# Kernel optimization log

Measured on AMD Instinct MI355X. Metric: run time of the kernel, lower is better.

The kernel has to match this reference:

```python
import jax, jax.numpy as jnp
import numpy as np

B, S, D, H = 2, 2048, 1024, 16
HD = D // H
EPS = 1e-8
LN_EPS = 1e-5


def setup_inputs() -> dict:
    key = jax.random.key(0)
    ks = jax.random.split(key, 12)
    std = 0.02
    inp = {}
    inp["x"] = jax.random.normal(ks[0], (B, S, D), jnp.float32)
    # q/k/v/out projections (stored (in, out); y = x @ W + b)
    inp["Wq"] = jax.random.normal(ks[1], (D, D), jnp.float32) * std
    inp["bq"] = jnp.zeros((D,), jnp.float32)
    inp["Wk"] = jax.random.normal(ks[2], (D, D), jnp.float32) * std
    inp["bk"] = jnp.zeros((D,), jnp.float32)
    inp["Wv"] = jax.random.normal(ks[3], (D, D), jnp.float32) * std
    inp["bv"] = jnp.zeros((D,), jnp.float32)
    inp["Wo"] = jax.random.normal(ks[4], (D, D), jnp.float32) * std
    inp["bo"] = jnp.zeros((D,), jnp.float32)
    # 4 DeltaResidualBlocks stacked on axis 0: [q, k, v, out]
    inp["dWk"] = jax.random.normal(ks[5], (4, D, D), jnp.float32) * 0.01  # k_proj, no bias
    inp["dbw"] = jnp.zeros((4, D), jnp.float32)                           # beta_proj weight (init zeros)
    inp["dbb"] = jnp.full((4,), -4.0, jnp.float32)                        # beta_proj bias
    inp["dWv"] = jax.random.normal(ks[6], (4, D), jnp.float32) * 0.02     # v_proj weight (d_v=1)
    inp["dbv"] = jnp.zeros((4,), jnp.float32)                             # v_proj bias
    inp["ln_g"] = jnp.ones((D,), jnp.float32)
    inp["ln_b"] = jnp.zeros((D,), jnp.float32)
    return inp


def reference(x, Wq, bq, Wk, bk, Wv, bv, Wo, bo, dWk, dbw, dbb, dWv, dbv, ln_g, ln_b):
    def delta(h, v_in, i):
        # DeltaResidualBlock (d_v=1): h + beta * k * (v - k.h)
        k_raw = jnp.einsum('bsd,de->bse', h, dWk[i])
        k = k_raw / (jnp.linalg.norm(k_raw, axis=-1, keepdims=True) + EPS)
        beta = 2.0 * jax.nn.sigmoid(jnp.einsum('bsd,d->bs', h, dbw[i])[..., None] + dbb[i])  # (B,S,1)
        v = jnp.einsum('bsd,d->bs', v_in, dWv[i])[..., None] + dbv[i]                        # (B,S,1)
        k_dot_h = jnp.sum(k * h, axis=-1, keepdims=True)
        return h + beta * k * (v - k_dot_h)

    q = delta(x, x @ Wq + bq, 0)
    k = delta(x, x @ Wk + bk, 1)
    v = delta(x, x @ Wv + bv, 2)

    # (B,S,D) -> (B,H,S,HD)
    q = q.reshape(B, S, H, HD).transpose(0, 2, 1, 3)
    k = k.reshape(B, S, H, HD).transpose(0, 2, 1, 3)
    v = v.reshape(B, S, H, HD).transpose(0, 2, 1, 3)

    scale = HD ** -0.5
    scores = jnp.einsum('bhqd,bhkd->bhqk', q, k) * scale
    attn = jax.nn.softmax(scores, axis=-1)
    out = jnp.einsum('bhqk,bhkd->bhqd', attn, v)
    out = out.transpose(0, 2, 1, 3).reshape(B, S, D)
    out = out @ Wo + bo

    y = delta(x, out, 3)

    # LayerNorm
    mu = jnp.mean(y, axis=-1, keepdims=True)
    var = jnp.mean((y - mu) ** 2, axis=-1, keepdims=True)
    y = (y - mu) / jnp.sqrt(var + LN_EPS) * ln_g + ln_b
    return y
```

## Files before the change

### kernel.cpp

```cpp
#include <hip/hip_runtime.h>

#define BB 2
#define SS 2048
#define DD 1024
#define HH 16
#define HD 64
#define MM (BB*SS)
#define KC 4
#define KT_PER (SS/64/KC)

typedef unsigned short u16;
typedef __attribute__((ext_vector_type(8))) short bf16x8;
typedef __attribute__((ext_vector_type(4))) float f32x4;

typedef __attribute__((address_space(1))) const unsigned int* gas_t;
typedef __attribute__((address_space(3))) unsigned int* las_t;

#ifndef __has_builtin
#define __has_builtin(x) 0
#endif
#if __has_builtin(__builtin_amdgcn_exp2f)
#define EXP2F(x) __builtin_amdgcn_exp2f(x)
#else
#define EXP2F(x) __expf((x)*0.6931471805599453f)
#endif
#define QSCALE 0.18033688011112042f

__device__ __forceinline__ void gl_lds16(const u16* g, u16* l){
  __builtin_amdgcn_global_load_lds((gas_t)g, (las_t)l, 16, 0, 0);
}

__device__ __forceinline__ u16 f2bf(float f){
  unsigned u = __float_as_uint(f);
  u += 0x7FFF + ((u >> 16) & 1);
  return (u16)(u >> 16);
}
__device__ __forceinline__ float bf2f(u16 h){
  return __uint_as_float(((unsigned)h) << 16);
}
__device__ __forceinline__ float dot4f(float4 a, float4 b){
  return a.x*b.x + a.y*b.y + a.z*b.z + a.w*b.w;
}

#define NB_CONV 2048
#define NB_TRAN 2048
#define NB_PREC 4100
#define NB_PREP (NB_CONV+NB_TRAN+NB_PREC)
__global__ void prep_kernel(const float* __restrict__ x, u16* __restrict__ xb,
                            const float* __restrict__ dWk, u16* __restrict__ dWkT,
                            const float* __restrict__ Wq_, const float* __restrict__ bq_,
                            const float* __restrict__ Wk_, const float* __restrict__ bk_,
                            const float* __restrict__ Wv_, const float* __restrict__ bv_,
                            const float* __restrict__ Wo_, const float* __restrict__ bo_,
                            const float* __restrict__ dWv, const float* __restrict__ dbv,
                            float* __restrict__ wv, float* __restrict__ cv) {
  int blk = blockIdx.x, t = threadIdx.x;
  if (blk < NB_CONV) {
    size_t idx = ((size_t)blk*256 + t)*8;
    float4 a = *(const float4*)(x + idx);
    float4 b = *(const float4*)(x + idx + 4);
    union { u16 u[8]; uint4 v; } pk;
    pk.u[0]=f2bf(a.x); pk.u[1]=f2bf(a.y); pk.u[2]=f2bf(a.z); pk.u[3]=f2bf(a.w);
    pk.u[4]=f2bf(b.x); pk.u[5]=f2bf(b.y); pk.u[6]=f2bf(b.z); pk.u[7]=f2bf(b.w);
    *(uint4*)(xb + idx) = pk.v;
    return;
  }
  blk -= NB_CONV;
  if (blk < NB_TRAN) {
    int xi = blk & 3, rest = blk >> 2;
    int ck = rest & 127, i = rest >> 7;
    int n  = xi*256 + t;
    const float* src = dWk + (size_t)i*DD*DD + (size_t)ck*8*DD + n;
    union { u16 u[8]; uint4 v; } pk;
    #pragma unroll
    for (int e=0;e<8;e++) pk.u[e] = f2bf(src[(size_t)e*DD]);
    *(uint4*)(dWkT + (size_t)i*DD*DD + (size_t)n*DD + ck*8) = pk.v;
    return;
  }
  blk -= NB_TRAN;
  {
    int i = blk / 1025, row = blk % 1025;
    const float* W    = (i==0)?Wq_:(i==1)?Wk_:(i==2)?Wv_:Wo_;
    const float* bvec = (i==0)?bq_:(i==1)?bk_:(i==2)?bv_:bo_;
    const float* s = dWv + i*DD;
    __shared__ float red[256];
    float acc = 0.f;
    if (row < DD) {
      const float* r = W + (size_t)row * DD;
      for (int e = t; e < DD; e += 256) acc += r[e]*s[e];
    } else {
      for (int e = t; e < DD; e += 256) acc += bvec[e]*s[e];
    }
    red[t] = acc; __syncthreads();
    for (int off=128; off>0; off>>=1){ if(t<off) red[t]+=red[t+off]; __syncthreads(); }
    if (t==0) {
      if (row < DD) wv[i*DD + row] = red[0];
      else          cv[i] = red[0] + dbv[i];
    }
  }
}

__global__ __launch_bounds__(256) void gemm_dwk_mfma(const u16* __restrict__ xb,
                          const u16* __restrict__ Bt, u16* __restrict__ kraw) {
  const int id = blockIdx.x;
  const int xcd = id & 7, j = id >> 3;
  const int i = j & 3, rest = j >> 2;
  const int mloc = rest & 7, nloc = rest >> 3;
  const int m0 = ((((xcd & 3) << 3) | mloc) << 7);
  const int n0 = ((((xcd >> 2) << 2) | nloc) << 7);
  const u16* Bm = Bt + (size_t)i*DD*DD;
  u16* C = kraw + (size_t)i*MM*DD;
  const int t = threadIdx.x, w = t>>6, lane = t&63;
  const int q15 = lane&15, quad = lane>>4;
  const int wm = w>>1, wn = w&1;
  const int lr = lane>>3, lc = lane&7, gsw = lc ^ lr;
  const int sw = q15 & 7;
  __shared__ u16 As[128*64];
  __shared__ u16 Bs[128*64];
  f32x4 acc[4][4];
  #pragma unroll
  for(int a=0;a<4;a++)
    #pragma unroll
    for(int b2=0;b2<4;b2++) acc[a][b2] = (f32x4){0.f,0.f,0.f,0.f};

  for (int k0=0; k0<DD; k0+=64) {
    __syncthreads();
    #pragma unroll
    for (int j2=0; j2<4; j2++) {
      int r = (w*4+j2)*8 + lr;
      gl_lds16(xb + (size_t)(m0+r)*DD + k0 + gsw*8, &As[((w*4+j2)*8)*64]);
      gl_lds16(Bm + (size_t)(n0+r)*DD + k0 + gsw*8, &Bs[((w*4+j2)*8)*64]);
    }
    __syncthreads();
    #pragma unroll
    for (int kk=0; kk<2; kk++) {
      bf16x8 af[4], bfr[4];
      #pragma unroll
      for (int mt=0; mt<4; mt++)
        af[mt]  = *(bf16x8*)(&As[(wm*64+mt*16+q15)*64 + ((kk*4+quad)^sw)*8]);
      #pragma unroll
      for (int nt=0; nt<4; nt++)
        bfr[nt] = *(bf16x8*)(&Bs[(wn*64+nt*16+q15)*64 + ((kk*4+quad)^sw)*8]);
      #pragma unroll
      for (int mt=0; mt<4; mt++)
        #pragma unroll
        for (int nt=0; nt<4; nt++)
          acc[mt][nt] = __builtin_amdgcn_mfma_f32_16x16x32_bf16(af[mt], bfr[nt], acc[mt][nt], 0,0,0);
    }
  }
  #pragma unroll
  for (int mt=0; mt<4; mt++)
    #pragma unroll
    for (int nt=0; nt<4; nt++)
      #pragma unroll
      for (int r=0; r<4; r++) {
        int m = m0 + wm*64 + mt*16 + quad*4 + r;
        int n = n0 + wn*64 + nt*16 + q15;
        C[(size_t)m*DD + n] = f2bf(acc[mt][nt][r]);
      }
}

__global__ void delta_qkv_kernel(const float* __restrict__ x, const u16* __restrict__ kraw,
                                 const float* __restrict__ dbw, const float* __restrict__ dbb,
                                 const float* __restrict__ wv, const float* __restrict__ cv,
                                 u16* __restrict__ qk, float* __restrict__ Vw) {
  int m = blockIdx.x, t = threadIdx.x, w = t>>6, lane = t&63;
  const float* xr = x + (size_t)m*DD;
  float4 xv = *(const float4*)(xr + t*4);
  __shared__ float4 part[3][4];
  float4 kvs[3];
  #pragma unroll
  for (int i=0;i<3;i++) {
    ushort4 ku = *(const ushort4*)(kraw + (size_t)i*MM*DD + (size_t)m*DD + t*4);
    float4 kv = make_float4(bf2f(ku.x), bf2f(ku.y), bf2f(ku.z), bf2f(ku.w));
    kvs[i] = kv;
    float4 bwv = *(const float4*)(dbw + i*DD + t*4);
    float4 wvv = *(const float4*)(wv  + i*DD + t*4);
    float4 red = make_float4(dot4f(kv,kv), dot4f(kv,xv), dot4f(xv,bwv), dot4f(xv,wvv));
    #pragma unroll
    for (int off=32; off>0; off>>=1) {
      red.x += __shfl_xor(red.x, off);
      red.y += __shfl_xor(red.y, off);
      red.z += __shfl_xor(red.z, off);
      red.w += __shfl_xor(red.w, off);
    }
    if (lane==0) part[i][w] = red;
  }
  __syncthreads();
  float cc[3];
  #pragma unroll
  for (int i=0;i<3;i++) {
    float4 r0=part[i][0], r1=part[i][1], r2=part[i][2], r3=part[i][3];
    float s0=r0.x+r1.x+r2.x+r3.x, s1=r0.y+r1.y+r2.y+r3.y;
    float s2=r0.z+r1.z+r2.z+r3.z, s3=r0.w+r1.w+r2.w+r3.w;
    float nrmE = sqrtf(s0) + 1e-8f;
    float kdh  = s1 / nrmE;
    float beta = 2.f / (1.f + __expf(-(s2 + dbb[i])));
    float vs   = s3 + cv[i];
    cc[i] = beta * (vs - kdh) / nrmE;
  }
  {
    float c = cc[0]; float4 kv = kvs[0];
    ushort4 ou;
    ou.x = f2bf((xv.x + c*kv.x)*QSCALE); ou.y = f2bf((xv.y + c*kv.y)*QSCALE);
    ou.z = f2bf((xv.z + c*kv.z)*QSCALE); ou.w = f2bf((xv.w + c*kv.w)*QSCALE);
    *(ushort4*)(qk + (size_t)m*DD + t*4) = ou;
  }
  {
    float c = cc[1]; float4 kv = kvs[1];
    ushort4 ou;
    ou.x = f2bf(xv.x + c*kv.x); ou.y = f2bf(xv.y + c*kv.y);
    ou.z = f2bf(xv.z + c*kv.z); ou.w = f2bf(xv.w + c*kv.w);
    *(ushort4*)(qk + (size_t)MM*DD + (size_t)m*DD + t*4) = ou;
  }
  {
    float c = cc[2]; float4 kv = kvs[2];
    float4 vv = make_float4(xv.x + c*kv.x, xv.y + c*kv.y, xv.z + c*kv.z, xv.w + c*kv.w);
    float4 w3 = *(const float4*)(wv + 3*DD + t*4);
    float s = dot4f(vv, w3);
    #pragma unroll
    for (int off=1; off<16; off<<=1) s += __shfl_xor(s, off);
    if ((lane & 15) == 0) {
      int head = t >> 4;
      int b = m >> 11, srow = m & (SS-1);
      Vw[((size_t)(b*HH + head))*SS + srow] = s;
    }
  }
}

__global__ __launch_bounds__(256) void flash_mfma(const u16* __restrict__ qb,
     const u16* __restrict__ kb, const float* __restrict__ Vw,
     float* __restrict__ l_arr, float* __restrict__ pv_arr) {
  const int qt = blockIdx.x, h = blockIdx.y;
  const int b = blockIdx.z >> 2, kc = blockIdx.z & 3;
  const int t = threadIdx.x, w = t>>6, lane = t&63, q15 = lane&15, quad = lane>>4;
  const int lr = lane>>3, lc = lane&7, gsw = lc ^ lr;
  const int sw = q15 & 7;
  __shared__ u16 Qs[64*64];
  __shared__ u16 Ks[2][64*64];
  const size_t hb = (size_t)h*HD;
  const u16* kbase = kb + (size_t)(b*SS + kc*KT_PER*64)*DD + hb;
  const float* vwb = Vw + (size_t)(b*HH + h)*SS + kc*KT_PER*64;

  #pragma unroll
  for (int j=0; j<2; j++) {
    int r = (w*2+j)*8 + lr;
    gl_lds16(qb + (size_t)(b*SS + qt*64 + r)*DD + hb + gsw*8, &Qs[((w*2+j)*8)*64]);
    gl_lds16(kbase + (size_t)r*DD + gsw*8, &Ks[0][((w*2+j)*8)*64]);
  }
  float4 vwreg[4];
  #pragma unroll
  for (int rt=0; rt<4; rt++) vwreg[rt] = *(const float4*)(vwb + rt*16 + quad*4);

  float l_acc = 0.f, pv_acc = 0.f;
  __syncthreads();
  bf16x8 qf[2];
  #pragma unroll
  for (int kk=0; kk<2; kk++)
    qf[kk] = *(bf16x8*)(&Qs[(w*16+q15)*64 + ((kk*4+quad)^sw)*8]);

  for (int kt=0; kt<KT_PER; kt++) {
    if (kt+1 < KT_PER) {
      #pragma unroll
      for (int j=0; j<2; j++) {
        int r = (w*2+j)*8 + lr;
        gl_lds16(kbase + (size_t)((kt+1)*64 + r)*DD + gsw*8,
                 &Ks[(kt+1)&1][((w*2+j)*8)*64]);
      }
    }
    f32x4 Sacc[4];
    #pragma unroll
    for (int rt=0; rt<4; rt++) Sacc[rt] = (f32x4){0.f,0.f,0.f,0.f};
    #pragma unroll
    for (int kk=0; kk<2; kk++) {
      #pragma unroll
      for (int rt=0; rt<4; rt++) {
        bf16x8 kf = *(bf16x8*)(&Ks[kt&1][(rt*16+q15)*64 + ((kk*4+quad)^sw)*8]);
        Sacc[rt] = __builtin_amdgcn_mfma_f32_16x16x32_bf16(kf, qf[kk], Sacc[rt], 0,0,0);
      }
    }
    float4 vwcur[4];
    #pragma unroll
    for (int rt=0; rt<4; rt++) vwcur[rt] = vwreg[rt];
    if (kt+1 < KT_PER) {
      #pragma unroll
      for (int rt=0; rt<4; rt++)
        vwreg[rt] = *(const float4*)(vwb + (kt+1)*64 + rt*16 + quad*4);
    }
    #pragma unroll
    for (int rt=0; rt<4; rt++) {
      float va[4] = {vwcur[rt].x, vwcur[rt].y, vwcur[rt].z, vwcur[rt].w};
      #pragma unroll
      for (int r=0; r<4; r++) {
        float p = EXP2F(fminf(Sacc[rt][r], 30.f));
        l_acc  += p;
        pv_acc += p * va[r];
      }
    }
    __syncthreads();
  }
  l_acc  += __shfl_xor(l_acc, 16);  l_acc  += __shfl_xor(l_acc, 32);
  pv_acc += __shfl_xor(pv_acc, 16); pv_acc += __shfl_xor(pv_acc, 32);
  if (quad == 0) {
    int tok = b*SS + qt*64 + w*16 + q15;
    size_t idx = ((size_t)kc*MM + tok)*HH + h;
    l_arr[idx]  = l_acc;
    pv_arr[idx] = pv_acc;
  }
}

__global__ void final_kernel(const float* __restrict__ x, const u16* __restrict__ kraw3,
                             const float* __restrict__ l_arr, const float* __restrict__ pv_arr,
                             const float* __restrict__ dbw, const float* __restrict__ dbb,
                             const float* __restrict__ cv,
                             const float* __restrict__ ln_g, const float* __restrict__ ln_b,
                             float* __restrict__ out) {
  int m = blockIdx.x, t = threadIdx.x, w = t>>6, lane = t&63;
  const float* xr = x     + (size_t)m*DD;
  const u16*   kr = kraw3 + (size_t)m*DD;
  float4 xv  = *(const float4*)(xr + t*4);
  ushort4 ku = *(const ushort4*)(kr + t*4);
  float4 kv  = make_float4(bf2f(ku.x), bf2f(ku.y), bf2f(ku.z), bf2f(ku.w));
  float4 bwv = *(const float4*)(dbw + 3*DD + t*4);
  __shared__ float4 part[4];
  __shared__ float2 part2[4];
  __shared__ float v3s;
  if (t < 16) {
    float lsum = 0.f, psum = 0.f;
    #pragma unroll
    for (int kc=0; kc<KC; kc++) {
      size_t idx = ((size_t)kc*MM + m)*HH + t;
      lsum += l_arr[idx];
      psum += pv_arr[idx];
    }
    float val = psum / lsum;
    #pragma unroll
    for (int off=1; off<16; off<<=1) val += __shfl_xor(val, off);
    if (t==0) v3s = val;
  }
  float4 red = make_float4(dot4f(kv,kv), dot4f(kv,xv), dot4f(xv,bwv), 0.f);
  #pragma unroll
  for (int off=32; off>0; off>>=1) {
    red.x += __shfl_xor(red.x, off);
    red.y += __shfl_xor(red.y, off);
    red.z += __shfl_xor(red.z, off);
  }
  if (lane==0) part[w] = red;
  __syncthreads();
  float4 r0=part[0], r1=part[1], r2=part[2], r3=part[3];
  float s0=r0.x+r1.x+r2.x+r3.x, s1=r0.y+r1.y+r2.y+r3.y, s2=r0.z+r1.z+r2.z+r3.z;
  float nrmE = sqrtf(s0) + 1e-8f;
  float kdh  = s1 / nrmE;
  float beta = 2.f / (1.f + __expf(-(s2 + dbb[3])));
  float v3   = v3s + cv[3];
  float c = beta * (v3 - kdh) / nrmE;
  float y0 = xv.x + c*kv.x, y1 = xv.y + c*kv.y, y2 = xv.z + c*kv.z, y3 = xv.w + c*kv.w;
  float2 rr = make_float2(y0+y1+y2+y3, y0*y0+y1*y1+y2*y2+y3*y3);
  #pragma unroll
  for (int off=32; off>0; off>>=1) {
    rr.x += __shfl_xor(rr.x, off);
    rr.y += __shfl_xor(rr.y, off);
  }
  if (lane==0) part2[w] = rr;
  __syncthreads();
  float ssum = part2[0].x+part2[1].x+part2[2].x+part2[3].x;
  float ssq  = part2[0].y+part2[1].y+part2[2].y+part2[3].y;
  float mu   = ssum * (1.f/DD);
  float var  = ssq * (1.f/DD) - mu*mu;
  float rstd = rsqrtf(var + 1e-5f);
  float4 g  = *(const float4*)(ln_g + t*4);
  float4 bb = *(const float4*)(ln_b + t*4);
  float4 ov;
  ov.x = (y0-mu)*rstd*g.x + bb.x;
  ov.y = (y1-mu)*rstd*g.y + bb.y;
  ov.z = (y2-mu)*rstd*g.z + bb.z;
  ov.w = (y3-mu)*rstd*g.w + bb.w;
  *(float4*)(out + (size_t)m*DD + t*4) = ov;
}

extern "C" void kernel_launch(void* const* d_in, const int* in_sizes, int n_in,
                              void* d_out, int out_size, void* d_ws, size_t ws_size,
                              hipStream_t stream) {
  const float* x    = (const float*)d_in[0];
  const float* Wq_  = (const float*)d_in[1];
  const float* bq_  = (const float*)d_in[2];
  const float* Wk_  = (const float*)d_in[3];
  const float* bk_  = (const float*)d_in[4];
  const float* Wv_  = (const float*)d_in[5];
  const float* bv_  = (const float*)d_in[6];
  const float* Wo_  = (const float*)d_in[7];
  const float* bo_  = (const float*)d_in[8];
  const float* dWk  = (const float*)d_in[9];
  const float* dbw  = (const float*)d_in[10];
  const float* dbb  = (const float*)d_in[11];
  const float* dWv  = (const float*)d_in[12];
  const float* dbv  = (const float*)d_in[13];
  const float* ln_g = (const float*)d_in[14];
  const float* ln_b = (const float*)d_in[15];
  float* out = (float*)d_out;
  char* WS = (char*)d_ws;

  float* wv     = (float*)WS;
  float* cv     = (float*)(WS + 16384);
  u16*   kraw   = (u16*)  (WS + 16640);
  u16*   qk     = (u16*)  (WS + 16640 + (size_t)4*MM*DD*2);
  u16*   dWkT   = (u16*)  (WS + 16640 + (size_t)6*MM*DD*2);
  u16*   xb     = (u16*)  (WS + 16640 + (size_t)6*MM*DD*2 + (size_t)4*DD*DD*2);
  char*  tail   = WS + 16640 + (size_t)6*MM*DD*2 + (size_t)8*DD*DD*2;
  float* Vw     = (float*)tail;
  float* l_arr  = (float*)(tail + (size_t)BB*HH*SS*4);
  float* pv_arr = (float*)(tail + (size_t)BB*HH*SS*4 + (size_t)KC*MM*HH*4);

  prep_kernel<<<NB_PREP, 256, 0, stream>>>(
      x, xb, dWk, dWkT, Wq_,bq_,Wk_,bk_,Wv_,bv_,Wo_,bo_, dWv, dbv, wv, cv);
  gemm_dwk_mfma<<<1024, 256, 0, stream>>>(xb, dWkT, kraw);
  delta_qkv_kernel<<<MM, 256, 0, stream>>>(x, kraw, dbw, dbb, wv, cv, qk, Vw);
  flash_mfma<<<dim3(SS/64, HH, BB*KC), 256, 0, stream>>>(
      qk, qk + (size_t)MM*DD, Vw, l_arr, pv_arr);
  final_kernel<<<MM, 256, 0, stream>>>(x, kraw + 3*(size_t)MM*DD, l_arr, pv_arr,
                                       dbw, dbb, cv, ln_g, ln_b, out);
}
```

Measured before the change: 236.7 us.

## Rewrite delta-key GEMM as 256x256 tile, double-buffered 8-phase pipelined kernel

Replaces the 128x128, single-buffered delta k_proj GEMM with a 256x256 tile kernel using 512 threads and two LDS buffers. Global-to-LDS loads for later k-steps are issued in halves between four MFMA phases, with explicit vmcnt waits, scheduling barriers and setprio to overlap memory with matrix math. The larger tile raises data reuse, and the grid shrinks to 256 blocks with a new XCD-aware mapping. This costs much more LDS and register pressure, leaves fewer blocks for load balancing, and relies on hand-tuned wait counts being correct.

```diff
diff --git a/kernel.cpp b/kernel.cpp
--- a/kernel.cpp
+++ b/kernel.cpp
@@ -8,6 +8,7 @@
 #define MM (BB*SS)
 #define KC 4
 #define KT_PER (SS/64/KC)
+#define KSTEPS (DD/64)
 
 typedef unsigned short u16;
 typedef __attribute__((ext_vector_type(8))) short bf16x8;
@@ -41,6 +42,12 @@
 __device__ __forceinline__ float dot4f(float4 a, float4 b){
   return a.x*b.x + a.y*b.y + a.z*b.z + a.w*b.w;
 }
+
+#define SBAR() do { \
+  __builtin_amdgcn_sched_barrier(0); \
+  __builtin_amdgcn_s_barrier(); \
+  __builtin_amdgcn_sched_barrier(0); \
+} while (0)
 
 #define NB_CONV 2048
 #define NB_TRAN 2048
@@ -100,63 +107,128 @@
   }
 }
 
-__global__ __launch_bounds__(256) void gemm_dwk_mfma(const u16* __restrict__ xb,
+
+__device__ __forceinline__ void stage_half(const u16* __restrict__ g, u16* l,
+                                           int k0, int half, int isA,
+                                           int wid, int lane) {
+  const int lr = lane>>3, lc = lane&7;
+  #pragma unroll
+  for (int j=0; j<2; j++) {
+    const int u = wid*2 + j;
+    int grow;
+    if (isA) grow = ((u & 8) ? 128 + ((u & 7)<<3) : (u<<3)) + (half<<6);
+    else     grow = ((u>>2)<<6) + ((u&3)<<3) + (half<<5);
+    gl_lds16(g + (size_t)(grow + lr)*DD + k0 + ((lc^lr)<<3), l + grow*64);
+  }
+}
+
+__device__ __forceinline__ void lda4(const u16* base, int row0, int q15, int quad,
+                                     int sw, bf16x8 (&f)[4][2]) {
+  #pragma unroll
+  for (int mf=0; mf<4; mf++)
+    #pragma unroll
+    for (int kk=0; kk<2; kk++)
+      f[mf][kk] = *(const bf16x8*)(base + (row0 + mf*16 + q15)*64 + (((kk*4+quad)^sw)<<3));
+}
+__device__ __forceinline__ void ldb2(const u16* base, int row0, int q15, int quad,
+                                     int sw, bf16x8 (&f)[2][2]) {
+  #pragma unroll
+  for (int nf=0; nf<2; nf++)
+    #pragma unroll
+    for (int kk=0; kk<2; kk++)
+      f[nf][kk] = *(const bf16x8*)(base + (row0 + nf*16 + q15)*64 + (((kk*4+quad)^sw)<<3));
+}
+__device__ __forceinline__ void quad_mfma(const bf16x8 (&af)[4][2], const bf16x8 (&bfr)[2][2],
+                                          f32x4 (&acc)[8][4], int mo, int no) {
+  __builtin_amdgcn_s_setprio(1);
+  #pragma unroll
+  for (int kk=0; kk<2; kk++)
+    #pragma unroll
+    for (int mf=0; mf<4; mf++)
+      #pragma unroll
+      for (int nf=0; nf<2; nf++)
+        acc[mo+mf][no+nf] = __builtin_amdgcn_mfma_f32_16x16x32_bf16(
+            af[mf][kk], bfr[nf][kk], acc[mo+mf][no+nf], 0,0,0);
+  __builtin_amdgcn_s_setprio(0);
+}
+
+__global__ __launch_bounds__(512, 2) void gemm_dwk_8ph(const u16* __restrict__ xb,
                           const u16* __restrict__ Bt, u16* __restrict__ kraw) {
-  const int id = blockIdx.x;
-  const int xcd = id & 7, j = id >> 3;
-  const int i = j & 3, rest = j >> 2;
-  const int mloc = rest & 7, nloc = rest >> 3;
-  const int m0 = ((((xcd & 3) << 3) | mloc) << 7);
-  const int n0 = ((((xcd >> 2) << 2) | nloc) << 7);
-  const u16* Bm = Bt + (size_t)i*DD*DD;
+  const int bid = blockIdx.x;
+  const int xcd = bid & 7, rr = bid >> 3;
+  const int i = xcd >> 1;
+  const int mt = ((xcd & 1) << 3) | (rr & 7);
+  const int ntile = rr >> 3;
+  const int m0 = mt << 8, n0 = ntile << 8;
+  const u16* Ab = xb + (size_t)m0*DD;
+  const u16* Bb = Bt + (size_t)i*DD*DD + (size_t)n0*DD;
   u16* C = kraw + (size_t)i*MM*DD;
-  const int t = threadIdx.x, w = t>>6, lane = t&63;
-  const int q15 = lane&15, quad = lane>>4;
-  const int wm = w>>1, wn = w&1;
-  const int lr = lane>>3, lc = lane&7, gsw = lc ^ lr;
-  const int sw = q15 & 7;
-  __shared__ u16 As[128*64];
-  __shared__ u16 Bs[128*64];
-  f32x4 acc[4][4];
-  #pragma unroll
-  for(int a=0;a<4;a++)
-    #pragma unroll
-    for(int b2=0;b2<4;b2++) acc[a][b2] = (f32x4){0.f,0.f,0.f,0.f};
-
-  for (int k0=0; k0<DD; k0+=64) {
-    __syncthreads();
-    #pragma unroll
-    for (int j2=0; j2<4; j2++) {
-      int r = (w*4+j2)*8 + lr;
-      gl_lds16(xb + (size_t)(m0+r)*DD + k0 + gsw*8, &As[((w*4+j2)*8)*64]);
-      gl_lds16(Bm + (size_t)(n0+r)*DD + k0 + gsw*8, &Bs[((w*4+j2)*8)*64]);
-    }
-    __syncthreads();
-    #pragma unroll
-    for (int kk=0; kk<2; kk++) {
-      bf16x8 af[4], bfr[4];
-      #pragma unroll
-      for (int mt=0; mt<4; mt++)
-        af[mt]  = *(bf16x8*)(&As[(wm*64+mt*16+q15)*64 + ((kk*4+quad)^sw)*8]);
-      #pragma unroll
-      for (int nt=0; nt<4; nt++)
-        bfr[nt] = *(bf16x8*)(&Bs[(wn*64+nt*16+q15)*64 + ((kk*4+quad)^sw)*8]);
-      #pragma unroll
-      for (int mt=0; mt<4; mt++)
-        #pragma unroll
-        for (int nt=0; nt<4; nt++)
-          acc[mt][nt] = __builtin_amdgcn_mfma_f32_16x16x32_bf16(af[mt], bfr[nt], acc[mt][nt], 0,0,0);
-    }
-  }
-  #pragma unroll
-  for (int mt=0; mt<4; mt++)
-    #pragma unroll
-    for (int nt=0; nt<4; nt++)
-      #pragma unroll
-      for (int r=0; r<4; r++) {
-        int m = m0 + wm*64 + mt*16 + quad*4 + r;
-        int n = n0 + wn*64 + nt*16 + q15;
-        C[(size_t)m*DD + n] = f2bf(acc[mt][nt][r]);
+
+  const int t = threadIdx.x, wid = t>>6, lane = t&63;
+  const int q15 = lane&15, quad = lane>>4, sw = q15&7;
+  const int wm = wid>>2, wn = wid&3;
+  const int arow = wm<<7, brow = wn<<6;
+
+  __shared__ u16 As[2][256*64];
+  __shared__ u16 Bs[2][256*64];
+
+  f32x4 acc[8][4];
+  #pragma unroll
+  for (int a=0;a<8;a++)
+    #pragma unroll
+    for (int b2=0;b2<4;b2++) acc[a][b2] = (f32x4){0.f,0.f,0.f,0.f};
+
+  stage_half(Ab, As[0], 0,  0, 1, wid, lane);
+  stage_half(Bb, Bs[0], 0,  0, 0, wid, lane);
+  stage_half(Bb, Bs[0], 0,  1, 0, wid, lane);
+  stage_half(Ab, As[0], 0,  1, 1, wid, lane);
+  stage_half(Ab, As[1], 64, 0, 1, wid, lane);
+  stage_half(Bb, Bs[1], 64, 0, 0, wid, lane);
+  stage_half(Bb, Bs[1], 64, 1, 0, wid, lane);
+  __builtin_amdgcn_sched_barrier(0);
+  asm volatile("s_waitcnt vmcnt(6)" ::: "memory");
+  SBAR();
+
+  for (int u=0; u<KSTEPS; ++u) {
+    const int cur = u & 1;
+    const u16* Ac = As[cur]; const u16* Bc = Bs[cur];
+    const int k1 = (u+1 < KSTEPS ? u+1 : KSTEPS-1) << 6;
+    const int k2 = (u+2 < KSTEPS ? u+2 : KSTEPS-1) << 6;
+    bf16x8 a0[4][2], a1[4][2], b0[2][2], b1[2][2];
+
+    lda4(Ac, arow,      q15, quad, sw, a0);
+    ldb2(Bc, brow,      q15, quad, sw, b0);
+    stage_half(Ab, As[cur^1], k1, 1, 1, wid, lane);
+    SBAR();
+    quad_mfma(a0, b0, acc, 0, 0);
+    SBAR();
+    ldb2(Bc, brow+32,   q15, quad, sw, b1);
+    stage_half(Ab, As[cur], k2, 0, 1, wid, lane);
+    SBAR();
+    quad_mfma(a0, b1, acc, 0, 2);
+    SBAR();
+    lda4(Ac, arow+64,   q15, quad, sw, a1);
+    stage_half(Bb, Bs[cur], k2, 0, 0, wid, lane);
+    SBAR();
+    quad_mfma(a1, b1, acc, 4, 2);
+    SBAR();
+    stage_half(Bb, Bs[cur], k2, 1, 0, wid, lane);
+    __builtin_amdgcn_sched_barrier(0);
+    asm volatile("s_waitcnt vmcnt(6)" ::: "memory");
+    SBAR();
+    quad_mfma(a1, b0, acc, 4, 0);
+    SBAR();
+  }
+
+  #pragma unroll
+  for (int mf=0; mf<8; mf++)
+    #pragma unroll
+    for (int nf=0; nf<4; nf++)
+      #pragma unroll
+      for (int r4=0; r4<4; r4++) {
+        int m = m0 + arow + mf*16 + quad*4 + r4;
+        int n = n0 + brow + nf*16 + q15;
+        C[(size_t)m*DD + n] = f2bf(acc[mf][nf][r4]);
       }
 }
 
@@ -413,7 +485,7 @@
 
   prep_kernel<<<NB_PREP, 256, 0, stream>>>(
       x, xb, dWk, dWkT, Wq_,bq_,Wk_,bk_,Wv_,bv_,Wo_,bo_, dWv, dbv, wv, cv);
-  gemm_dwk_mfma<<<1024, 256, 0, stream>>>(xb, dWkT, kraw);
+  gemm_dwk_8ph<<<256, 512, 0, stream>>>(xb, dWkT, kraw);
   delta_qkv_kernel<<<MM, 256, 0, stream>>>(x, kraw, dbw, dbb, wv, cv, qk, Vw);
   flash_mfma<<<dim3(SS/64, HH, BB*KC), 256, 0, stream>>>(
       qk, qk + (size_t)MM*DD, Vw, l_arr, pv_arr);
```

Result: faster. 230.6 us (-2.6%).
